# Performance work log

Hardware: AMD Instinct MI355X
Metric: run time of the kernel (lower is better)

Reference implementation:

```python
import jax, jax.numpy as jnp
import numpy as np

DIM = 128
EDGE_COUNT = 128
N_NODES = 128
GRAPH_COUNT = 8
VOCAB = 100000
VEC_DIM = 300


def setup_inputs():
    key = jax.random.key(0)
    ks = jax.random.split(key, 8)
    rng = np.random.default_rng(0)
    data = jnp.asarray(rng.integers(0, VOCAB, size=N_NODES), dtype=jnp.int32)
    types = jnp.zeros((N_NODES,), dtype=jnp.int32)  # single data_type
    edges = jnp.asarray(rng.integers(0, EDGE_COUNT, size=N_NODES), dtype=jnp.int32)
    # parent-offset trees: node i's parent is a node > i, last node is the single root (offset 0)
    g = np.zeros((GRAPH_COUNT, N_NODES), dtype=np.int32)
    for j in range(GRAPH_COUNT):
        for i in range(N_NODES - 1):
            p = int(rng.integers(i + 1, N_NODES))
            g[j, i] = p - i
    graphs = jnp.asarray(g)
    inv_sqrt_d = 1.0 / np.sqrt(DIM)
    inv_sqrt_v = 1.0 / np.sqrt(VEC_DIM)
    return {
        "data": data, "types": types, "graphs": graphs, "edges": edges, "pos": 37,
        "data_vecs": jax.random.normal(ks[0], (VOCAB, VEC_DIM), jnp.float32),
        "data_weights": jax.random.normal(ks[1], (VEC_DIM, DIM), jnp.float32) * inv_sqrt_v,
        "data_biases": jax.random.normal(ks[2], (DIM,), jnp.float32) * 0.1,
        "edge_weights": jax.random.normal(ks[3], (EDGE_COUNT, DIM, DIM), jnp.float32) * inv_sqrt_d,
        "edge_biases": jax.random.normal(ks[4], (EDGE_COUNT, DIM), jnp.float32) * 0.1,
        "score_embedding_weights": jax.random.normal(ks[5], (DIM, 1), jnp.float32) * inv_sqrt_d,
        "score_data_weights": jax.random.normal(ks[6], (DIM, 1), jnp.float32) * inv_sqrt_d,
        "score_bias": jax.random.normal(ks[7], (1, 1), jnp.float32),
    }


def _tree_structure(parents_row):
    # Faithful reproduction of calc_embedding's structure handling (numpy on int constants).
    parents = np.asarray(parents_row).copy()
    n = len(parents)
    roots = [i for i in range(n) if parents[i] == 0]
    for i in range(len(roots) - 1):
        parents[roots[i]] = roots[i + 1]
    root = roots[-1]
    parents[root] = -n
    children = {}
    for i in range(n):
        pp = i + int(parents[i])
        children.setdefault(pp, []).append(i)
    order = []  # DFS preorder from root; reversed gives children-before-parent
    stack = [root]
    while stack:
        node = stack.pop()
        order.append(node)
        stack.extend(children.get(node, []))
    return root, children, order


def _forward(data, types, graphs, edges, pos,
             data_vecs, data_weights, data_biases,
             edge_weights, edge_biases,
             score_embedding_weights, score_data_weights, score_bias):
    data_np = np.asarray(data)
    graphs_np = np.asarray(graphs)
    edges_np = np.asarray(edges).copy()
    E, D, _ = edge_weights.shape
    # data embedding + data score for the queried position
    d_emb = data_vecs[data_np[pos]] @ data_weights + data_biases          # (D,)
    d_score = score_bias[0, 0] + d_emb @ score_data_weights[:, 0]         # scalar
    edges_np[pos] = -1  # unknown edge at pos -> branch over all edge types
    # base embeddings for all nodes at once: (N, D)
    base = data_vecs[data_np] @ data_weights + data_biases

    def transform(child_emb, eid):
        # child_emb: (E, D). eid < 0 -> per-edge-type weights (baddbmm over all E edges)
        if eid < 0:
            return jnp.einsum('ed,edk->ek', child_emb, edge_weights) + edge_biases
        return child_emb @ edge_weights[eid] + edge_biases[eid]

    scores = []
    for j in range(graphs_np.shape[0]):
        root, children, order = _tree_structure(graphs_np[j])
        emb = {}
        for n in reversed(order):  # children before parents
            e = jnp.broadcast_to(base[n], (E, D))
            ch = children.get(n, [])
            for c in ch:
                e = e + transform(emb.pop(c), int(edges_np[c]))
            if ch:
                e = jax.nn.relu(e)  # clamp(min=0) only for internal nodes
            emb[n] = e
        res = transform(emb[root], int(edges_np[root]))  # add_child_embedding(zeros, root_emb, edges[root])
        scores.append(d_score + res @ score_embedding_weights[:, 0])  # (E,)
    return jnp.stack(scores)  # (GRAPH_COUNT, EDGE_COUNT)


def reference(data, types, graphs, edges, pos, data_vecs, data_weights, data_biases,
              edge_weights, edge_biases, score_embedding_weights, score_data_weights, score_bias):
    return _forward(data, types, graphs, edges, pos, data_vecs, data_weights, data_biases,
                    edge_weights, edge_biases, score_embedding_weights, score_data_weights, score_bias)
```

## Files before the change

### kernel.cpp

```cpp
#include <hip/hip_runtime.h>
#include <stdint.h>


#define NND 128
#define DD  128
#define GG  8
#define VD  300
#define CH  4

typedef unsigned int u32;

#define F_RELU (1u<<16)
#define F_POS  (1u<<17)
#define F_PATH (1u<<18)

#define SYNC_LDS() asm volatile("s_waitcnt lgkmcnt(0)\n\ts_barrier" ::: "memory")

__global__ void __launch_bounds__(128) k_base(
        const int* __restrict__ data, const int* __restrict__ posArr,
        const float* __restrict__ vecs, const float* __restrict__ dw,
        const float* __restrict__ db,   const float* __restrict__ sdw,
        const float* __restrict__ sb,
        float* __restrict__ base, float* __restrict__ dscore)
{
    __shared__ __align__(16) float row[VD];
    __shared__ float red[DD];
    int n = blockIdx.x, t = threadIdx.x;
    int id = data[n];
    const float4* vp = (const float4*)(vecs + (size_t)id * VD);
    for (int i = t; i < VD/4; i += 128) ((float4*)row)[i] = vp[i];
    __syncthreads();
    float acc = db[t];
    for (int d = 0; d < VD; ++d)
        acc = fmaf(row[d], dw[d*DD + t], acc);
    base[n*DD + t] = acc;
    if (n == posArr[0]){
        red[t] = acc * sdw[t];
        __syncthreads();
        for (int o = 64; o > 0; o >>= 1){ if (t < o) red[t] += red[t+o]; __syncthreads(); }
        if (t == 0) dscore[0] = sb[0] + red[0];
    }
}

__global__ void __launch_bounds__(256, 1) k_tree(
        const int* __restrict__ graphs, const int* __restrict__ edges,
        const int* __restrict__ posArr, const float* __restrict__ EW,
        const float* __restrict__ EB,   const float* __restrict__ base,
        float* __restrict__ vposG, float* __restrict__ uG, int* __restrict__ meta)
{
    __shared__ __align__(16) float acc[NND-1][DD];
    __shared__ u32 desc[NND];
    int g = blockIdx.x, t = threadIdx.x;

    for (int idx = t; idx < (NND-1)*DD/4; idx += 256)
        ((float4*)acc)[idx] = ((const float4*)(base + DD))[idx];

    int myPar = -1;
    if (t < NND){
        myPar = (t < NND-1) ? (t + graphs[g*NND + t]) : 0;
        desc[t] = (u32)(myPar & 0xFF) | ((u32)edges[t] << 8);
    }
    __syncthreads();
    if (t < NND-1) atomicOr(&desc[myPar], F_RELU);
    if (t == 0){
        int p = posArr[0];
        atomicOr(&desc[p], F_POS);
        int c = desc[p] & 0xFF;
        int s = 0;
        for (;;){
            atomicOr(&desc[c], F_PATH | ((u32)s << 24));
            meta[g*(NND+1) + 1 + s] = c;
            ++s;
            if (c == NND-1) break;
            c = desc[c] & 0xFF;
        }
        meta[g*(NND+1)] = s;
    }
    __syncthreads();

    int l = t & 63, w = t >> 6;
    int k4 = w*8 + (l & 7);
    int d0 = (l >> 3) * 16;
    bool owner = ((l >> 3) == 0);

    auto pfW = [&](int edge, float4 (&wr)[16], float4& ebr){
        const float* Wp = EW + (size_t)edge*(DD*DD) + (size_t)d0*DD + 4*k4;
        #pragma unroll
        for (int d = 0; d < 16; ++d) wr[d] = *(const float4*)&Wp[d*DD];
        ebr = *(const float4*)&EB[(size_t)edge*DD + 4*k4];
    };

    auto stepGo = [&](int i, float4 (&wr)[16], float4& ebr, int iPf){
        u32 dsc = desc[i];
        const float* src = (i == 0) ? base : &acc[i-1][0];
        if (dsc & (F_POS | F_PATH)){
            if (dsc & F_POS){
                if (t < DD){
                    float v = src[t];
                    if (dsc & F_RELU) v = fmaxf(v, 0.f);
                    vposG[g*DD + t] = v;
                }
            } else {
                int slot = (int)(dsc >> 24);
                if (t < DD) uG[((size_t)g*NND + slot)*DD + t] = src[t];
            }
        } else {
            int par = (int)(dsc & 0xFF);
            float ev[16];
            #pragma unroll
            for (int j = 0; j < 4; ++j){
                float4 x = *(const float4*)&src[d0 + 4*j];
                ev[4*j+0]=x.x; ev[4*j+1]=x.y; ev[4*j+2]=x.z; ev[4*j+3]=x.w;
            }
            if (dsc & F_RELU){
                #pragma unroll
                for (int j = 0; j < 16; ++j) ev[j] = fmaxf(ev[j], 0.f);
            }
            float s0=0.f, s1=0.f, s2=0.f, s3=0.f;
            #pragma unroll
            for (int d = 0; d < 16; ++d){
                s0 = fmaf(ev[d], wr[d].x, s0);
                s1 = fmaf(ev[d], wr[d].y, s1);
                s2 = fmaf(ev[d], wr[d].z, s2);
                s3 = fmaf(ev[d], wr[d].w, s3);
            }
            #pragma unroll
            for (int m = 8; m <= 32; m <<= 1){
                s0 += __shfl_xor(s0, m);
                s1 += __shfl_xor(s1, m);
                s2 += __shfl_xor(s2, m);
                s3 += __shfl_xor(s3, m);
            }
            if (owner){
                float4* dst = (float4*)&acc[par-1][4*k4];
                float4 o = *dst;
                o.x += s0 + ebr.x; o.y += s1 + ebr.y;
                o.z += s2 + ebr.z; o.w += s3 + ebr.w;
                *dst = o;
            }
        }
        if (iPf < NND){
            int eN = (int)((desc[iPf] >> 8) & 0xFF);
            pfW(eN, wr, ebr);
        }
        SYNC_LDS();
    };

    float4 wA[16], wB[16], ebA, ebB;
    { int e0 = (int)((desc[0] >> 8) & 0xFF); pfW(e0, wA, ebA); }
    { int e1 = (int)((desc[1] >> 8) & 0xFF); pfW(e1, wB, ebB); }
    for (int ii = 0; ii < NND; ii += 2){
        stepGo(ii,     wA, ebA, ii+2);
        stepGo(ii + 1, wB, ebB, ii+3);
    }
}

__global__ void __launch_bounds__(256, 1) k_chain(
        const int* __restrict__ edges,
        const float* __restrict__ EW, const float* __restrict__ EB,
        const float* __restrict__ SEW,
        const float* __restrict__ vposG, const float* __restrict__ uG,
        const int* __restrict__ meta, const float* __restrict__ dscore,
        float* __restrict__ outp)
{
    __shared__ __align__(16) float Vbuf[2][CH][DD];
    __shared__ float red[CH][4];
    int g = blockIdx.x >> 5, chunk = blockIdx.x & 31;
    int t = threadIdx.x, l = t & 63, w = t >> 6;
    int k4 = w*8 + (l & 7);
    int d0 = (l >> 3) * 16;
    bool owner = ((l >> 3) == 0);
    int eBase = chunk * CH;
    int L = meta[g*(NND+1)];

    float vpf[16];
    #pragma unroll
    for (int j = 0; j < 4; ++j){
        float4 x = *(const float4*)&vposG[g*DD + d0 + 4*j];
        vpf[4*j+0]=x.x; vpf[4*j+1]=x.y; vpf[4*j+2]=x.z; vpf[4*j+3]=x.w;
    }
    float4 u0 = *(const float4*)&uG[(size_t)g*NND*DD + 4*k4];

    #pragma unroll 2
    for (int p = 0; p < CH; ++p){
        int e = eBase + p;
        const float* Wp = EW + (size_t)e*(DD*DD) + (size_t)d0*DD + 4*k4;
        float s0=0.f, s1=0.f, s2=0.f, s3=0.f;
        #pragma unroll
        for (int d = 0; d < 16; ++d){
            float4 wv = *(const float4*)&Wp[d*DD];
            s0 = fmaf(vpf[d], wv.x, s0);
            s1 = fmaf(vpf[d], wv.y, s1);
            s2 = fmaf(vpf[d], wv.z, s2);
            s3 = fmaf(vpf[d], wv.w, s3);
        }
        #pragma unroll
        for (int m = 8; m <= 32; m <<= 1){
            s0 += __shfl_xor(s0, m); s1 += __shfl_xor(s1, m);
            s2 += __shfl_xor(s2, m); s3 += __shfl_xor(s3, m);
        }
        if (owner){
            float4 bb = *(const float4*)&EB[(size_t)e*DD + 4*k4];
            float4 r;
            r.x = fmaxf(u0.x + s0 + bb.x, 0.f);
            r.y = fmaxf(u0.y + s1 + bb.y, 0.f);
            r.z = fmaxf(u0.z + s2 + bb.z, 0.f);
            r.w = fmaxf(u0.w + s3 + bb.w, 0.f);
            *(float4*)&Vbuf[0][p][4*k4] = r;
        }
    }
    __syncthreads();

    int cur = 0;
    for (int s = 1; s < L; ++s){
        int pn = meta[g*(NND+1) + s];
        int ej = edges[pn];
        const float* Wp = EW + (size_t)ej*(DD*DD) + (size_t)d0*DD + 4*k4;
        float4 wr[16];
        #pragma unroll
        for (int d = 0; d < 16; ++d) wr[d] = *(const float4*)&Wp[d*DD];
        float4 us = *(const float4*)&uG[((size_t)g*NND + s)*DD + 4*k4];
        float4 bb = *(const float4*)&EB[(size_t)ej*DD + 4*k4];
        #pragma unroll
        for (int p = 0; p < CH; ++p){
            float ev[16];
            #pragma unroll
            for (int j = 0; j < 4; ++j){
                float4 x = *(const float4*)&Vbuf[cur][p][d0 + 4*j];
                ev[4*j+0]=x.x; ev[4*j+1]=x.y; ev[4*j+2]=x.z; ev[4*j+3]=x.w;
            }
            float s0=0.f, s1=0.f, s2=0.f, s3=0.f;
            #pragma unroll
            for (int d = 0; d < 16; ++d){
                s0 = fmaf(ev[d], wr[d].x, s0);
                s1 = fmaf(ev[d], wr[d].y, s1);
                s2 = fmaf(ev[d], wr[d].z, s2);
                s3 = fmaf(ev[d], wr[d].w, s3);
            }
            #pragma unroll
            for (int m = 8; m <= 32; m <<= 1){
                s0 += __shfl_xor(s0, m); s1 += __shfl_xor(s1, m);
                s2 += __shfl_xor(s2, m); s3 += __shfl_xor(s3, m);
            }
            if (owner){
                float4 r;
                r.x = fmaxf(us.x + s0 + bb.x, 0.f);
                r.y = fmaxf(us.y + s1 + bb.y, 0.f);
                r.z = fmaxf(us.z + s2 + bb.z, 0.f);
                r.w = fmaxf(us.w + s3 + bb.w, 0.f);
                *(float4*)&Vbuf[cur^1][p][4*k4] = r;
            }
        }
        __syncthreads();
        cur ^= 1;
    }

    {
        int rn = meta[g*(NND+1) + L];
        int er = edges[rn];
        const float* Wp = EW + (size_t)er*(DD*DD) + (size_t)d0*DD + 4*k4;
        float4 wr[16];
        #pragma unroll
        for (int d = 0; d < 16; ++d) wr[d] = *(const float4*)&Wp[d*DD];
        float4 bb = *(const float4*)&EB[(size_t)er*DD + 4*k4];
        float4 sw = *(const float4*)&SEW[4*k4];
        #pragma unroll
        for (int p = 0; p < CH; ++p){
            float ev[16];
            #pragma unroll
            for (int j = 0; j < 4; ++j){
                float4 x = *(const float4*)&Vbuf[cur][p][d0 + 4*j];
                ev[4*j+0]=x.x; ev[4*j+1]=x.y; ev[4*j+2]=x.z; ev[4*j+3]=x.w;
            }
            float s0=0.f, s1=0.f, s2=0.f, s3=0.f;
            #pragma unroll
            for (int d = 0; d < 16; ++d){
                s0 = fmaf(ev[d], wr[d].x, s0);
                s1 = fmaf(ev[d], wr[d].y, s1);
                s2 = fmaf(ev[d], wr[d].z, s2);
                s3 = fmaf(ev[d], wr[d].w, s3);
            }
            #pragma unroll
            for (int m = 8; m <= 32; m <<= 1){
                s0 += __shfl_xor(s0, m); s1 += __shfl_xor(s1, m);
                s2 += __shfl_xor(s2, m); s3 += __shfl_xor(s3, m);
            }
            if (owner){
                float part = (s0 + bb.x) * sw.x + (s1 + bb.y) * sw.y
                           + (s2 + bb.z) * sw.z + (s3 + bb.w) * sw.w;
                part += __shfl_xor(part, 1);
                part += __shfl_xor(part, 2);
                part += __shfl_xor(part, 4);
                if (l == 0) red[p][w] = part;
            }
        }
        __syncthreads();
        if (t < CH)
            outp[g*DD + eBase + t] = dscore[0] + red[t][0] + red[t][1] + red[t][2] + red[t][3];
    }
}

extern "C" void kernel_launch(void* const* d_in, const int* in_sizes, int n_in,
                              void* d_out, int out_size, void* d_ws, size_t ws_size,
                              hipStream_t stream)
{
    const int*   data   = (const int*)d_in[0];
    const int*   graphs = (const int*)d_in[2];
    const int*   edges  = (const int*)d_in[3];
    const int*   posArr = (const int*)d_in[4];
    const float* vecs   = (const float*)d_in[5];
    const float* dw     = (const float*)d_in[6];
    const float* db     = (const float*)d_in[7];
    const float* ew     = (const float*)d_in[8];
    const float* eb     = (const float*)d_in[9];
    const float* sew    = (const float*)d_in[10];
    const float* sdw    = (const float*)d_in[11];
    const float* sb     = (const float*)d_in[12];

    char* ws = (char*)d_ws;
    float* base   = (float*)(ws);
    float* vposG  = (float*)(ws + 65536);
    float* uG     = (float*)(ws + 65536 + 4096);
    float* dscore = (float*)(ws + 65536 + 4096 + 524288);
    int*   meta   = (int*)  (ws + 65536 + 4096 + 524288 + 256);

    float* outp = (float*)d_out;

    k_base <<<NND, 128, 0, stream>>>(data, posArr, vecs, dw, db, sdw, sb, base, dscore);
    k_tree <<<GG, 256, 0, stream>>>(graphs, edges, posArr, ew, eb, base, vposG, uG, meta);
    k_chain<<<GG*(DD/CH), 256, 0, stream>>>(edges, ew, eb, sew, vposG, uG, meta, dscore, outp);
}
```

Baseline: 346.2 us.

## Process tree nodes level-by-level in parallel instead of sequentially

Replaces the sequential 128-step node walk in k_tree with a level-synchronous schedule. Node depths come from pointer jumping, nodes are bucketed by level, and each wavefront of a 1024-thread block processes one node per level, gathering child contributions from a CSR child list. This cuts the serial chain of barriers from one per node to one per tree level, but drops the double-buffered weight prefetch and adds setup work with O(n) scans. k_base also gets four independent accumulators to break its FMA dependency chain.

```diff
diff --git a/kernel.cpp b/kernel.cpp
--- a/kernel.cpp
+++ b/kernel.cpp
@@ -10,11 +10,8 @@
 
 typedef unsigned int u32;
 
-#define F_RELU (1u<<16)
-#define F_POS  (1u<<17)
-#define F_PATH (1u<<18)
-
-#define SYNC_LDS() asm volatile("s_waitcnt lgkmcnt(0)\n\ts_barrier" ::: "memory")
+#define F_POS  (1<<16)
+#define F_PATH (1<<17)
 
 __global__ void __launch_bounds__(128) k_base(
         const int* __restrict__ data, const int* __restrict__ posArr,
@@ -30,9 +27,14 @@
     const float4* vp = (const float4*)(vecs + (size_t)id * VD);
     for (int i = t; i < VD/4; i += 128) ((float4*)row)[i] = vp[i];
     __syncthreads();
-    float acc = db[t];
-    for (int d = 0; d < VD; ++d)
-        acc = fmaf(row[d], dw[d*DD + t], acc);
+    float a0 = db[t], a1 = 0.f, a2 = 0.f, a3 = 0.f;
+    for (int d = 0; d < VD; d += 4){
+        a0 = fmaf(row[d+0], dw[(d+0)*DD + t], a0);
+        a1 = fmaf(row[d+1], dw[(d+1)*DD + t], a1);
+        a2 = fmaf(row[d+2], dw[(d+2)*DD + t], a2);
+        a3 = fmaf(row[d+3], dw[(d+3)*DD + t], a3);
+    }
+    float acc = (a0 + a1) + (a2 + a3);
     base[n*DD + t] = acc;
     if (n == posArr[0]){
         red[t] = acc * sdw[t];
@@ -42,116 +44,134 @@
     }
 }
 
-__global__ void __launch_bounds__(256, 1) k_tree(
+__global__ void __launch_bounds__(1024, 1) k_tree(
         const int* __restrict__ graphs, const int* __restrict__ edges,
         const int* __restrict__ posArr, const float* __restrict__ EW,
         const float* __restrict__ EB,   const float* __restrict__ base,
         float* __restrict__ vposG, float* __restrict__ uG, int* __restrict__ meta)
 {
-    __shared__ __align__(16) float acc[NND-1][DD];
-    __shared__ u32 desc[NND];
+    __shared__ __align__(16) float contrib[NND-1][DD];
+    __shared__ int par_s[NND], eid_s[NND], flg_s[NND];
+    __shared__ int ccnt[NND], cstart[NND], cidx[NND];
+    __shared__ int dep[NND], anc[NND], lcnt[NND], lstart[NND], order[NND];
+    __shared__ int maxD_s;
+
     int g = blockIdx.x, t = threadIdx.x;
 
-    for (int idx = t; idx < (NND-1)*DD/4; idx += 256)
-        ((float4*)acc)[idx] = ((const float4*)(base + DD))[idx];
-
-    int myPar = -1;
-    if (t < NND){
-        myPar = (t < NND-1) ? (t + graphs[g*NND + t]) : 0;
-        desc[t] = (u32)(myPar & 0xFF) | ((u32)edges[t] << 8);
-    }
-    __syncthreads();
-    if (t < NND-1) atomicOr(&desc[myPar], F_RELU);
+    if (t < NND){
+        par_s[t] = (t < NND-1) ? (t + graphs[g*NND + t]) : (NND-1);
+        eid_s[t] = edges[t];
+        flg_s[t] = 0;
+        ccnt[t]  = 0;
+        lcnt[t]  = 0;
+    }
+    if (t == 0) maxD_s = 0;
+    __syncthreads();
+
+    int mySlot = 0;
+    if (t < NND-1){
+        int p = par_s[t];
+        atomicAdd(&ccnt[p], 1);
+        for (int c = 0; c < t; ++c) mySlot += (par_s[c] == p);
+    }
+    if (t < NND){
+        dep[t] = (t < NND-1) ? 1 : 0;
+        anc[t] = par_s[t];
+    }
     if (t == 0){
         int p = posArr[0];
-        atomicOr(&desc[p], F_POS);
-        int c = desc[p] & 0xFF;
-        int s = 0;
+        flg_s[p] |= F_POS;
+        int c = par_s[p], s = 0;
         for (;;){
-            atomicOr(&desc[c], F_PATH | ((u32)s << 24));
+            flg_s[c] |= F_PATH | (s << 24);
             meta[g*(NND+1) + 1 + s] = c;
             ++s;
             if (c == NND-1) break;
-            c = desc[c] & 0xFF;
+            c = par_s[c];
         }
         meta[g*(NND+1)] = s;
     }
     __syncthreads();
 
-    int l = t & 63, w = t >> 6;
-    int k4 = w*8 + (l & 7);
-    int d0 = (l >> 3) * 16;
-    bool owner = ((l >> 3) == 0);
-
-    auto pfW = [&](int edge, float4 (&wr)[16], float4& ebr){
-        const float* Wp = EW + (size_t)edge*(DD*DD) + (size_t)d0*DD + 4*k4;
-        #pragma unroll
-        for (int d = 0; d < 16; ++d) wr[d] = *(const float4*)&Wp[d*DD];
-        ebr = *(const float4*)&EB[(size_t)edge*DD + 4*k4];
-    };
-
-    auto stepGo = [&](int i, float4 (&wr)[16], float4& ebr, int iPf){
-        u32 dsc = desc[i];
-        const float* src = (i == 0) ? base : &acc[i-1][0];
-        if (dsc & (F_POS | F_PATH)){
-            if (dsc & F_POS){
-                if (t < DD){
-                    float v = src[t];
-                    if (dsc & F_RELU) v = fmaxf(v, 0.f);
-                    vposG[g*DD + t] = v;
+    if (t < NND){
+        int s = 0;
+        for (int p = 0; p < t; ++p) s += ccnt[p];
+        cstart[t] = s;
+    }
+    __syncthreads();
+    if (t < NND-1) cidx[cstart[par_s[t]] + mySlot] = t;
+
+    for (int k = 0; k < 7; ++k){
+        int d2 = 0, a2 = 0;
+        if (t < NND){ d2 = dep[t] + dep[anc[t]]; a2 = anc[anc[t]]; }
+        __syncthreads();
+        if (t < NND){ dep[t] = d2; anc[t] = a2; }
+        __syncthreads();
+    }
+    if (t < NND) atomicMax(&maxD_s, dep[t]);
+    if (t < NND) atomicAdd(&lcnt[dep[t]], 1);
+    __syncthreads();
+
+    if (t < NND){
+        int s = 0;
+        for (int d2 = 0; d2 < t; ++d2) s += lcnt[d2];
+        lstart[t] = s;
+    }
+    __syncthreads();
+    if (t < NND){
+        int d2 = dep[t], s = 0;
+        for (int c = 0; c < t; ++c) s += (dep[c] == d2);
+        order[lstart[d2] + s] = t;
+    }
+    __syncthreads();
+
+    int w = t >> 6, l = t & 63;
+    int c0 = 2*l;
+    int maxD = maxD_s;
+
+    for (int d = maxD; d >= 0; --d){
+        int lo = lstart[d], cnt = lcnt[d];
+        for (int q = w; q < cnt; q += 16){
+            int n = order[lo + q];
+            float2 bse = *(const float2*)&base[n*DD + c0];
+            float e0 = bse.x, e1 = bse.y;
+            int cs = cstart[n], cc = ccnt[n];
+            for (int j = 0; j < cc; ++j){
+                int c = cidx[cs + j];
+                if (!(flg_s[c] & (F_POS | F_PATH))){
+                    float2 cv = *(const float2*)&contrib[c][c0];
+                    e0 += cv.x; e1 += cv.y;
                 }
+            }
+            int f = flg_s[n];
+            if (f & F_POS){
+                if (cc){ e0 = fmaxf(e0, 0.f); e1 = fmaxf(e1, 0.f); }
+                *(float2*)&vposG[g*DD + c0] = make_float2(e0, e1);
+            } else if (f & F_PATH){
+                int slot = ((u32)f) >> 24;
+                *(float2*)&uG[((size_t)g*NND + slot)*DD + c0] = make_float2(e0, e1);
             } else {
-                int slot = (int)(dsc >> 24);
-                if (t < DD) uG[((size_t)g*NND + slot)*DD + t] = src[t];
-            }
-        } else {
-            int par = (int)(dsc & 0xFF);
-            float ev[16];
-            #pragma unroll
-            for (int j = 0; j < 4; ++j){
-                float4 x = *(const float4*)&src[d0 + 4*j];
-                ev[4*j+0]=x.x; ev[4*j+1]=x.y; ev[4*j+2]=x.z; ev[4*j+3]=x.w;
-            }
-            if (dsc & F_RELU){
-                #pragma unroll
-                for (int j = 0; j < 16; ++j) ev[j] = fmaxf(ev[j], 0.f);
-            }
-            float s0=0.f, s1=0.f, s2=0.f, s3=0.f;
-            #pragma unroll
-            for (int d = 0; d < 16; ++d){
-                s0 = fmaf(ev[d], wr[d].x, s0);
-                s1 = fmaf(ev[d], wr[d].y, s1);
-                s2 = fmaf(ev[d], wr[d].z, s2);
-                s3 = fmaf(ev[d], wr[d].w, s3);
-            }
-            #pragma unroll
-            for (int m = 8; m <= 32; m <<= 1){
-                s0 += __shfl_xor(s0, m);
-                s1 += __shfl_xor(s1, m);
-                s2 += __shfl_xor(s2, m);
-                s3 += __shfl_xor(s3, m);
-            }
-            if (owner){
-                float4* dst = (float4*)&acc[par-1][4*k4];
-                float4 o = *dst;
-                o.x += s0 + ebr.x; o.y += s1 + ebr.y;
-                o.z += s2 + ebr.z; o.w += s3 + ebr.w;
-                *dst = o;
-            }
-        }
-        if (iPf < NND){
-            int eN = (int)((desc[iPf] >> 8) & 0xFF);
-            pfW(eN, wr, ebr);
-        }
-        SYNC_LDS();
-    };
-
-    float4 wA[16], wB[16], ebA, ebB;
-    { int e0 = (int)((desc[0] >> 8) & 0xFF); pfW(e0, wA, ebA); }
-    { int e1 = (int)((desc[1] >> 8) & 0xFF); pfW(e1, wB, ebB); }
-    for (int ii = 0; ii < NND; ii += 2){
-        stepGo(ii,     wA, ebA, ii+2);
-        stepGo(ii + 1, wB, ebB, ii+3);
+                if (cc){ e0 = fmaxf(e0, 0.f); e1 = fmaxf(e1, 0.f); }
+                *(float2*)&contrib[n][c0] = make_float2(e0, e1);
+                asm volatile("s_waitcnt lgkmcnt(0)" ::: "memory");
+                int e = eid_s[n];
+                const float* Wp = EW + (size_t)e*(DD*DD) + c0;
+                float s0a=0.f, s1a=0.f, s0b=0.f, s1b=0.f;
+                #pragma unroll 8
+                for (int dd = 0; dd < DD/2; ++dd){
+                    float x0 = contrib[n][dd];
+                    float x1 = contrib[n][DD/2 + dd];
+                    float2 w0 = *(const float2*)&Wp[(size_t)dd*DD];
+                    float2 w1 = *(const float2*)&Wp[(size_t)(DD/2+dd)*DD];
+                    s0a = fmaf(x0, w0.x, s0a); s1a = fmaf(x0, w0.y, s1a);
+                    s0b = fmaf(x1, w1.x, s0b); s1b = fmaf(x1, w1.y, s1b);
+                }
+                float2 bb = *(const float2*)&EB[(size_t)e*DD + c0];
+                *(float2*)&contrib[n][c0] = make_float2(s0a + s0b + bb.x,
+                                                        s1a + s1b + bb.y);
+            }
+        }
+        __syncthreads();
     }
 }
 
@@ -327,6 +347,6 @@
     float* outp = (float*)d_out;
 
     k_base <<<NND, 128, 0, stream>>>(data, posArr, vecs, dw, db, sdw, sb, base, dscore);
-    k_tree <<<GG, 256, 0, stream>>>(graphs, edges, posArr, ew, eb, base, vposG, uG, meta);
+    k_tree <<<GG, 1024, 0, stream>>>(graphs, edges, posArr, ew, eb, base, vposG, uG, meta);
     k_chain<<<GG*(DD/CH), 256, 0, stream>>>(edges, ew, eb, sew, vposG, uG, meta, dscore, outp);
 }
```

Measured after the change: 356.2 us. +2.9%, slower.
